# Performance work log

Measured on AMD Instinct MI355X. Metric: run time of the kernel, lower is better.

Reference implementation:

```python
import jax, jax.numpy as jnp
import numpy as np

NMS_RADIUS = 3       # conf.nms_radius (odd)
MAX_KPTS = 2048      # conf.max_num_keypoints
SUBPIXEL_TEMP = 0.5  # conf.subpixel_temp


def setup_inputs() -> dict:
    key = jax.random.key(0)
    k1, k2, k3 = jax.random.split(key, 3)
    B, H, W, C = 4, 640, 640, 64
    return {
        "keypoint_probs": jax.random.uniform(k1, (B, 1, H, W), dtype=jnp.float32),
        "raw_logits": jax.random.normal(k2, (B, 1, H, W), dtype=jnp.float32),
        "feature_map": jax.random.normal(k3, (B, C, H, W), dtype=jnp.float32),
    }


def _bilinear_sample(fm, x, y):
    # fm: (B,C,H,W); x,y: (B,N) pixel coords. F.grid_sample bilinear,
    # padding_mode='border', align_corners=True == clamp pixel coords then bilerp.
    B, C, H, W = fm.shape
    x = jnp.clip(x, 0.0, W - 1)
    y = jnp.clip(y, 0.0, H - 1)
    x0f = jnp.floor(x); y0f = jnp.floor(y)
    wx = (x - x0f)[:, None, :]
    wy = (y - y0f)[:, None, :]
    x0 = x0f.astype(jnp.int32); y0 = y0f.astype(jnp.int32)
    x1 = jnp.clip(x0 + 1, 0, W - 1); y1 = jnp.clip(y0 + 1, 0, H - 1)
    fm_flat = fm.reshape(B, C, H * W)
    bidx = jnp.arange(B)[:, None, None]
    def g(iy, ix):
        return fm_flat[bidx, jnp.arange(C)[None, :, None], (iy * W + ix)[:, None, :]]
    v00 = g(y0, x0); v01 = g(y0, x1); v10 = g(y1, x0); v11 = g(y1, x1)
    out = (v00 * (1 - wx) * (1 - wy) + v01 * wx * (1 - wy)
           + v10 * (1 - wx) * wy + v11 * wx * wy)      # (B,C,N)
    return out.transpose(0, 2, 1)                       # (B,N,C)


def reference(keypoint_probs, raw_logits, feature_map):
    B, _, H, W = keypoint_probs.shape
    r, K = NMS_RADIUS, MAX_KPTS
    pad = r // 2
    # --- NMS: keep only local maxima of the score map ---
    p = keypoint_probs[:, 0]                             # (B,H,W)
    maxp = jax.lax.reduce_window(p, -jnp.inf, jax.lax.max,
                                 (1, r, r), (1, 1, 1),
                                 ((0, 0), (pad, pad), (pad, pad)))
    nms = jnp.where(p == maxp, p, 0.0)
    # --- top-k keypoints over flattened H*W ---
    _, hw = jax.lax.top_k(nms.reshape(B, H * W), K)      # (B,K)
    h = hw // W
    w = hw % W
    kpts = jnp.stack([w, h], axis=-1).astype(jnp.float32)  # (x,y)
    # --- subpixel refinement: gather r*r patch of raw logits around each kp ---
    logits_pad = jnp.pad(raw_logits[:, 0], ((0, 0), (pad, pad), (pad, pad)))  # zero pad like nn.Unfold
    Wp = W + 2 * pad
    di, dj = jnp.meshgrid(jnp.arange(r), jnp.arange(r), indexing='ij')
    di = di.reshape(-1); dj = dj.reshape(-1)             # (r*r,)
    idx = (h[:, None, :] + di[None, :, None]) * Wp + (w[:, None, :] + dj[None, :, None])  # (B,r2,K)
    patches = logits_pad.reshape(B, -1)[jnp.arange(B)[:, None, None], idx]  # (B,r2,K)
    probs_patch = jax.nn.softmax(patches / SUBPIXEL_TEMP, axis=1)
    off = jnp.linspace(-(r - 1) / 2, (r - 1) / 2, r)
    gy, gx = jnp.meshgrid(off, off, indexing='ij')
    offsets = jnp.stack([gx, gy], axis=-1).reshape(r * r, 2).astype(jnp.float32)  # (x,y) order
    kpts = kpts + jnp.einsum('bkn,kd->bnd', probs_patch, offsets)
    # --- bilinear sample score map + descriptors at refined keypoints (one pass) ---
    stacked = jnp.concatenate([keypoint_probs, feature_map], axis=1)  # (B,1+C,H,W)
    sampled = _bilinear_sample(stacked, kpts[..., 0], kpts[..., 1])   # (B,K,1+C)
    # output: [x, y, score, desc...] per keypoint -> (B,K,2+1+C)
    return jnp.concatenate([kpts, sampled], axis=-1)
```

## Files before the change

### kernel.cpp

```cpp
#include <hip/hip_runtime.h>
#include <stdint.h>

#define B_ 4
#define H_ 640
#define W_ 640
#define C_ 64
#define K_ 2048
#define N_ (H_ * W_)
#define NBINS 131072
#define CAP 4096
#define CBLK 64
#define CHUNK (N_ / CBLK)

#define OFF_BITS   0
#define SZ_BITS    (B_ * N_ * 4)
#define OFF_HIST   (OFF_BITS + SZ_BITS)
#define SZ_HIST    (B_ * NBINS * 4)
#define OFF_CCNT   (OFF_HIST + SZ_HIST)
#define SZ_CCNT    256
#define OFF_BSTAR  (OFF_CCNT + SZ_CCNT)
#define SZ_BSTAR   16
#define OFF_CAND   (OFF_BSTAR + SZ_BSTAR)
#define SZ_CAND    (B_ * CAP * 8)
#define OFF_TOPK   (OFF_CAND + SZ_CAND)
#define SZ_TOPK    (B_ * K_ * 4)

__global__ void nms_hist_kernel(const float* __restrict__ p,
                                uint32_t* __restrict__ bits_out,
                                uint32_t* __restrict__ hist) {
    int t = blockIdx.x * blockDim.x + threadIdx.x;
    if (t >= B_ * N_) return;
    int b = t / N_;
    int i = t - b * N_;
    int y = i / W_;
    int x = i - y * W_;
    const float* pb = p + (size_t)b * N_;
    float c = pb[i];
    float m = c;
    #pragma unroll
    for (int dy = -1; dy <= 1; dy++) {
        int yy = y + dy;
        if (yy < 0 || yy >= H_) continue;
        #pragma unroll
        for (int dx = -1; dx <= 1; dx++) {
            int xx = x + dx;
            if (xx < 0 || xx >= W_) continue;
            m = fmaxf(m, pb[yy * W_ + xx]);
        }
    }
    float nms = (c == m) ? c : 0.0f;
    uint32_t bits = __float_as_uint(nms);
    bits_out[t] = bits;
    if (bits) atomicAdd(&hist[b * NBINS + (bits >> 13)], 1u);
}

__global__ __launch_bounds__(1024) void findbin_kernel(const uint32_t* __restrict__ hist,
                                                       uint32_t* __restrict__ binstar) {
    int b = blockIdx.x;
    const uint32_t* h = hist + b * NBINS;
    __shared__ uint32_t suf[1024];
    __shared__ uint32_t ssel, scum;
    int tid = threadIdx.x;
    uint32_t s = 0;
    int base = tid * 128;
    for (int j = 0; j < 128; j++) s += h[base + j];
    suf[tid] = s;
    if (tid == 0) ssel = 0xFFFFFFFFu;
    __syncthreads();
    for (int off = 1; off < 1024; off <<= 1) {
        uint32_t v = suf[tid];
        uint32_t add = (tid + off < 1024) ? suf[tid + off] : 0u;
        __syncthreads();
        suf[tid] = v + add;
        __syncthreads();
    }
    uint32_t inc = suf[tid];
    uint32_t above = inc - s;
    if (above < (uint32_t)K_ && inc >= (uint32_t)K_) { ssel = tid; scum = above; }
    __syncthreads();
    if (tid < 64) {
        uint32_t sel = ssel;
        if (sel != 0xFFFFFFFFu) {
            int b2 = sel * 128 + tid * 2;
            uint32_t c0 = h[b2], c1 = h[b2 + 1];
            uint32_t pair = c0 + c1;
            uint32_t acc = pair;
            #pragma unroll
            for (int off = 1; off < 64; off <<= 1) {
                uint32_t v = __shfl_down(acc, off);
                if (tid + off < 64) acc += v;
            }
            uint32_t aboveL = scum + (acc - pair);
            if (aboveL < (uint32_t)K_ && aboveL + pair >= (uint32_t)K_) {
                uint32_t bstar = (aboveL + c1 >= (uint32_t)K_) ? (uint32_t)(b2 + 1)
                                                               : (uint32_t)b2;
                binstar[b] = bstar;
            }
        } else if (tid == 0) {
            binstar[b] = 0;
        }
    }
}

__global__ __launch_bounds__(256) void collect_kernel(const uint32_t* __restrict__ bits_in,
                                                      const uint32_t* __restrict__ binstar,
                                                      uint32_t* __restrict__ ccnt,
                                                      unsigned long long* __restrict__ cand) {
    int b = blockIdx.x / CBLK;
    int c = blockIdx.x - b * CBLK;
    int base = b * N_ + c * CHUNK;
    uint32_t bstar = binstar[b];
    int tid = threadIdx.x;
    int lane = tid & 63, wv = tid >> 6;
    __shared__ uint32_t wtot[4];
    __shared__ uint32_t blkbase;

    uint32_t cnt = 0;
    for (int j = tid; j < CHUNK; j += 256) {
        uint32_t bits = bits_in[base + j];
        if (bits && (bits >> 13) >= bstar) cnt++;
    }
    #pragma unroll
    for (int off = 32; off > 0; off >>= 1) cnt += __shfl_down(cnt, off);
    if (lane == 0) wtot[wv] = cnt;
    __syncthreads();
    if (tid == 0) {
        uint32_t tot = wtot[0] + wtot[1] + wtot[2] + wtot[3];
        blkbase = tot ? atomicAdd(&ccnt[b * 16], tot) : 0u;
    }
    __syncthreads();
    uint32_t wbase = blkbase;
    #pragma unroll
    for (int w2 = 0; w2 < 4; w2++) if (w2 < wv) wbase += wtot[w2];

    uint32_t run = 0;
    for (int j = tid; j < CHUNK; j += 256) {
        uint32_t bits = bits_in[base + j];
        bool pass = bits && (bits >> 13) >= bstar;
        unsigned long long mask = __ballot(pass);
        if (pass) {
            uint32_t pos = wbase + run + (uint32_t)__popcll(mask & ((1ull << lane) - 1));
            int i = c * CHUNK + j;
            if (pos < CAP)
                cand[(size_t)b * CAP + pos] =
                    ((unsigned long long)bits << 32) | (unsigned long long)(0xFFFFFFFFu - (uint32_t)i);
        }
        run += (uint32_t)__popcll(mask);
    }
}

__global__ __launch_bounds__(1024) void sort_kernel(const unsigned long long* __restrict__ cand,
                                                    const uint32_t* __restrict__ ccnt,
                                                    uint32_t* __restrict__ topk) {
    __shared__ unsigned long long sh[CAP];
    int b = blockIdx.x;
    int tid = threadIdx.x;
    uint32_t cnt = ccnt[b * 16];
    if (cnt > CAP) cnt = CAP;
    const unsigned long long* cb = cand + (size_t)b * CAP;
    for (int j = tid; j < CAP; j += 1024) sh[j] = (j < (int)cnt) ? cb[j] : 0ULL;
    __syncthreads();
    for (unsigned k = 2; k <= CAP; k <<= 1) {
        for (unsigned j = k >> 1; j > 0; j >>= 1) {
            for (unsigned t = tid; t < CAP / 2; t += 1024) {
                unsigned i = (t / j) * (2 * j) + (t % j);
                unsigned ixj = i + j;
                unsigned long long a = sh[i], cc = sh[ixj];
                bool dirDesc = ((i & k) == 0);
                if (dirDesc ? (a < cc) : (a > cc)) { sh[i] = cc; sh[ixj] = a; }
            }
            __syncthreads();
        }
    }
    for (int k2 = tid; k2 < K_; k2 += 1024) {
        topk[b * K_ + k2] = 0xFFFFFFFFu - (uint32_t)(sh[k2] & 0xFFFFFFFFull);
    }
}

__global__ void final_kernel(const uint32_t* __restrict__ topk,
                             const float* __restrict__ probs,
                             const float* __restrict__ logits,
                             const float* __restrict__ fm,
                             float* __restrict__ out) {
    int gtid = blockIdx.x * blockDim.x + threadIdx.x;
    int wid = gtid >> 6;
    int lane = threadIdx.x & 63;
    if (wid >= B_ * K_) return;
    int b = wid / K_;
    int k = wid - b * K_;
    int idx = (int)topk[b * K_ + k];
    int h = idx / W_;
    int w = idx - h * W_;

    const float* lg = logits + (size_t)b * N_;
    float v[9];
    #pragma unroll
    for (int di = 0; di < 3; di++) {
        #pragma unroll
        for (int dj = 0; dj < 3; dj++) {
            int yy = h + di - 1, xx = w + dj - 1;
            float val = (yy >= 0 && yy < H_ && xx >= 0 && xx < W_) ? lg[yy * W_ + xx] : 0.0f;
            v[di * 3 + dj] = val * 2.0f;
        }
    }
    float m = v[0];
    #pragma unroll
    for (int j = 1; j < 9; j++) m = fmaxf(m, v[j]);
    float e[9], s = 0.0f;
    #pragma unroll
    for (int j = 0; j < 9; j++) { e[j] = __expf(v[j] - m); s += e[j]; }
    float inv = 1.0f / s;
    float dx = 0.0f, dy = 0.0f;
    #pragma unroll
    for (int di = 0; di < 3; di++) {
        #pragma unroll
        for (int dj = 0; dj < 3; dj++) {
            float pr = e[di * 3 + dj] * inv;
            dx += pr * (float)(dj - 1);
            dy += pr * (float)(di - 1);
        }
    }
    float x = (float)w + dx;
    float y = (float)h + dy;

    float xc = fminf(fmaxf(x, 0.0f), (float)(W_ - 1));
    float yc = fminf(fmaxf(y, 0.0f), (float)(H_ - 1));
    float x0f = floorf(xc), y0f = floorf(yc);
    float wx = xc - x0f, wy = yc - y0f;
    int x0 = (int)x0f, y0 = (int)y0f;
    int x1 = min(x0 + 1, W_ - 1), y1 = min(y0 + 1, H_ - 1);
    float w00 = (1.0f - wx) * (1.0f - wy);
    float w01 = wx * (1.0f - wy);
    float w10 = (1.0f - wx) * wy;
    float w11 = wx * wy;
    int i00 = y0 * W_ + x0, i01 = y0 * W_ + x1, i10 = y1 * W_ + x0, i11 = y1 * W_ + x1;

    float* ob = out + ((size_t)b * K_ + k) * (C_ + 3);

    const float* ch = fm + ((size_t)b * C_ + lane) * N_;
    float sv = ch[i00] * w00 + ch[i01] * w01 + ch[i10] * w10 + ch[i11] * w11;
    ob[3 + lane] = sv;

    if (lane == 0) {
        const float* pp = probs + (size_t)b * N_;
        float sp = pp[i00] * w00 + pp[i01] * w01 + pp[i10] * w10 + pp[i11] * w11;
        ob[0] = x;
        ob[1] = y;
        ob[2] = sp;
    }
}

extern "C" void kernel_launch(void* const* d_in, const int* in_sizes, int n_in,
                              void* d_out, int out_size, void* d_ws, size_t ws_size,
                              hipStream_t stream) {
    const float* probs  = (const float*)d_in[0];
    const float* logits = (const float*)d_in[1];
    const float* fm     = (const float*)d_in[2];
    float* out = (float*)d_out;

    char* ws = (char*)d_ws;
    uint32_t* bits   = (uint32_t*)(ws + OFF_BITS);
    uint32_t* hist   = (uint32_t*)(ws + OFF_HIST);
    uint32_t* ccnt   = (uint32_t*)(ws + OFF_CCNT);
    uint32_t* bstar  = (uint32_t*)(ws + OFF_BSTAR);
    unsigned long long* cand = (unsigned long long*)(ws + OFF_CAND);
    uint32_t* topk   = (uint32_t*)(ws + OFF_TOPK);

    hipMemsetAsync((void*)hist, 0, SZ_HIST + SZ_CCNT, stream);

    int total = B_ * N_;
    int blk = 256;
    nms_hist_kernel<<<(total + blk - 1) / blk, blk, 0, stream>>>(probs, bits, hist);
    findbin_kernel<<<B_, 1024, 0, stream>>>(hist, bstar);
    collect_kernel<<<B_ * CBLK, 256, 0, stream>>>(bits, bstar, ccnt, cand);
    sort_kernel<<<B_, 1024, 0, stream>>>(cand, ccnt, topk);

    int waves = B_ * K_;
    int threads = waves * 64;
    final_kernel<<<(threads + 255) / 256, 256, 0, stream>>>(topk, probs, logits, fm, out);
}
```

Measured before the change: 647.4 us.

## Vectorize NMS to four pixels per thread and restructure histogram bin search

The NMS/histogram kernel now handles four adjacent pixels per thread, reading float4 rows plus halo values and writing uint4 results. This cuts redundant neighbourhood loads and the thread count. The bin-finding kernel is rewritten as a three-level hierarchical search: segment sums read with vector loads, a wave-level scan with ballot, a 2048-bin segment staged into shared memory, then two wave scans. This replaces the serial 128-element per-thread loop and the long barrier-heavy block scan. The -1 padding sentinel is only correct because the probabilities are non-negative, and the code assumes W is divisible by four.

```diff
diff --git a/kernel.cpp b/kernel.cpp
--- a/kernel.cpp
+++ b/kernel.cpp
@@ -29,75 +29,140 @@
                                 uint32_t* __restrict__ bits_out,
                                 uint32_t* __restrict__ hist) {
     int t = blockIdx.x * blockDim.x + threadIdx.x;
-    if (t >= B_ * N_) return;
-    int b = t / N_;
-    int i = t - b * N_;
-    int y = i / W_;
-    int x = i - y * W_;
+    if (t >= B_ * N_ / 4) return;
+    int b = t / (N_ / 4);
+    int i4 = (t - b * (N_ / 4)) * 4;
+    int y = i4 / W_;
+    int x0 = i4 - y * W_;
     const float* pb = p + (size_t)b * N_;
-    float c = pb[i];
-    float m = c;
-    #pragma unroll
-    for (int dy = -1; dy <= 1; dy++) {
-        int yy = y + dy;
-        if (yy < 0 || yy >= H_) continue;
-        #pragma unroll
-        for (int dx = -1; dx <= 1; dx++) {
-            int xx = x + dx;
-            if (xx < 0 || xx >= W_) continue;
-            m = fmaxf(m, pb[yy * W_ + xx]);
-        }
-    }
-    float nms = (c == m) ? c : 0.0f;
-    uint32_t bits = __float_as_uint(nms);
-    bits_out[t] = bits;
-    if (bits) atomicAdd(&hist[b * NBINS + (bits >> 13)], 1u);
+
+    float4 rows[3];
+    float lft[3], rgt[3];
+    #pragma unroll
+    for (int r = 0; r < 3; r++) {
+        int yy = y + r - 1;
+        if (yy < 0 || yy >= H_) {
+            rows[r] = make_float4(-1.f, -1.f, -1.f, -1.f);
+            lft[r] = -1.f; rgt[r] = -1.f;
+        } else {
+            const float* rp = pb + yy * W_;
+            rows[r] = *(const float4*)(rp + x0);
+            lft[r] = (x0 > 0)       ? rp[x0 - 1] : -1.f;
+            rgt[r] = (x0 + 4 < W_)  ? rp[x0 + 4] : -1.f;
+        }
+    }
+    float m0 = -1.f, m1 = -1.f, m2 = -1.f, m3 = -1.f;
+    #pragma unroll
+    for (int r = 0; r < 3; r++) {
+        float4 v = rows[r];
+        m0 = fmaxf(m0, fmaxf(fmaxf(lft[r], v.x), v.y));
+        m1 = fmaxf(m1, fmaxf(fmaxf(v.x, v.y), v.z));
+        m2 = fmaxf(m2, fmaxf(fmaxf(v.y, v.z), v.w));
+        m3 = fmaxf(m3, fmaxf(fmaxf(v.z, v.w), rgt[r]));
+    }
+    float4 c = rows[1];
+    uint4 bits;
+    bits.x = (c.x == m0) ? __float_as_uint(c.x) : 0u;
+    bits.y = (c.y == m1) ? __float_as_uint(c.y) : 0u;
+    bits.z = (c.z == m2) ? __float_as_uint(c.z) : 0u;
+    bits.w = (c.w == m3) ? __float_as_uint(c.w) : 0u;
+    *(uint4*)(bits_out + (size_t)b * N_ + i4) = bits;
+
+    uint32_t* hb = hist + b * NBINS;
+    if (bits.x) atomicAdd(&hb[bits.x >> 13], 1u);
+    if (bits.y) atomicAdd(&hb[bits.y >> 13], 1u);
+    if (bits.z) atomicAdd(&hb[bits.z >> 13], 1u);
+    if (bits.w) atomicAdd(&hb[bits.w >> 13], 1u);
 }
 
 __global__ __launch_bounds__(1024) void findbin_kernel(const uint32_t* __restrict__ hist,
                                                        uint32_t* __restrict__ binstar) {
     int b = blockIdx.x;
     const uint32_t* h = hist + b * NBINS;
-    __shared__ uint32_t suf[1024];
-    __shared__ uint32_t ssel, scum;
+    __shared__ uint32_t segsum[64];
+    __shared__ uint32_t seg[2048];
+    __shared__ uint32_t s_sel, s_scum;
     int tid = threadIdx.x;
-    uint32_t s = 0;
-    int base = tid * 128;
-    for (int j = 0; j < 128; j++) s += h[base + j];
-    suf[tid] = s;
-    if (tid == 0) ssel = 0xFFFFFFFFu;
-    __syncthreads();
-    for (int off = 1; off < 1024; off <<= 1) {
-        uint32_t v = suf[tid];
-        uint32_t add = (tid + off < 1024) ? suf[tid + off] : 0u;
-        __syncthreads();
-        suf[tid] = v + add;
-        __syncthreads();
-    }
-    uint32_t inc = suf[tid];
-    uint32_t above = inc - s;
-    if (above < (uint32_t)K_ && inc >= (uint32_t)K_) { ssel = tid; scum = above; }
-    __syncthreads();
-    if (tid < 64) {
-        uint32_t sel = ssel;
-        if (sel != 0xFFFFFFFFu) {
-            int b2 = sel * 128 + tid * 2;
-            uint32_t c0 = h[b2], c1 = h[b2 + 1];
-            uint32_t pair = c0 + c1;
-            uint32_t acc = pair;
-            #pragma unroll
-            for (int off = 1; off < 64; off <<= 1) {
-                uint32_t v = __shfl_down(acc, off);
-                if (tid + off < 64) acc += v;
+    int lane = tid & 63, wv = tid >> 6;
+
+    #pragma unroll
+    for (int si = 0; si < 4; si++) {
+        int s = wv * 4 + si;
+        const uint32_t* sb = h + s * 2048;
+        uint32_t acc = 0;
+        #pragma unroll
+        for (int it = 0; it < 8; it++) {
+            uint4 v = *(const uint4*)(sb + (it * 64 + lane) * 4);
+            acc += v.x + v.y + v.z + v.w;
+        }
+        #pragma unroll
+        for (int off = 32; off > 0; off >>= 1) acc += __shfl_down(acc, off);
+        if (lane == 0) segsum[s] = acc;
+    }
+    __syncthreads();
+
+    if (wv == 0) {
+        uint32_t own = segsum[lane];
+        uint32_t inc = own;
+        #pragma unroll
+        for (int off = 1; off < 64; off <<= 1) {
+            uint32_t v = __shfl_down(inc, off);
+            if (lane + off < 64) inc += v;
+        }
+        uint32_t above = inc - own;
+        bool sel = (above < (uint32_t)K_) && (inc >= (uint32_t)K_);
+        unsigned long long msk = __ballot(sel);
+        if (lane == 0) {
+            if (msk == 0ULL) { s_sel = 0xFFFFFFFFu; }
+            else {
+                int s = __ffsll((long long)msk) - 1;
+                s_sel = (uint32_t)s;
             }
-            uint32_t aboveL = scum + (acc - pair);
-            if (aboveL < (uint32_t)K_ && aboveL + pair >= (uint32_t)K_) {
-                uint32_t bstar = (aboveL + c1 >= (uint32_t)K_) ? (uint32_t)(b2 + 1)
-                                                               : (uint32_t)b2;
-                binstar[b] = bstar;
-            }
-        } else if (tid == 0) {
-            binstar[b] = 0;
+        }
+        if (msk != 0ULL) {
+            int s = __ffsll((long long)msk) - 1;
+            uint32_t sc = __shfl(above, s);
+            if (lane == 0) s_scum = sc;
+        }
+    }
+    __syncthreads();
+
+    uint32_t selseg = s_sel;
+    if (selseg == 0xFFFFFFFFu) {
+        if (tid == 0) binstar[b] = 0;
+        return;
+    }
+    if (tid < 512) {
+        ((uint4*)seg)[tid] = ((const uint4*)(h + selseg * 2048))[tid];
+    }
+    __syncthreads();
+
+    if (wv == 0) {
+        uint32_t scum = s_scum;
+        uint32_t cs = 0;
+        #pragma unroll
+        for (int j = 0; j < 32; j++) cs += seg[lane * 32 + ((j + lane) & 31)];
+        uint32_t incc = cs;
+        #pragma unroll
+        for (int off = 1; off < 64; off <<= 1) {
+            uint32_t v = __shfl_down(incc, off);
+            if (lane + off < 64) incc += v;
+        }
+        uint32_t above2 = scum + (incc - cs);
+        bool sel2 = (above2 < (uint32_t)K_) && (above2 + cs >= (uint32_t)K_);
+        unsigned long long m2 = __ballot(sel2);
+        int cidx = __ffsll((long long)m2) - 1;
+        uint32_t scum2 = __shfl(above2, cidx);
+        uint32_t bv = (lane < 32) ? seg[cidx * 32 + lane] : 0u;
+        uint32_t incb = bv;
+        #pragma unroll
+        for (int off = 1; off < 32; off <<= 1) {
+            uint32_t v = __shfl_down(incb, off);
+            if (lane + off < 32) incb += v;
+        }
+        uint32_t above3 = scum2 + (incb - bv);
+        if (lane < 32 && above3 < (uint32_t)K_ && above3 + bv >= (uint32_t)K_) {
+            binstar[b] = (uint32_t)(selseg * 2048 + cidx * 32 + lane);
         }
     }
 }
@@ -268,9 +333,9 @@
 
     hipMemsetAsync((void*)hist, 0, SZ_HIST + SZ_CCNT, stream);
 
-    int total = B_ * N_;
     int blk = 256;
-    nms_hist_kernel<<<(total + blk - 1) / blk, blk, 0, stream>>>(probs, bits, hist);
+    int total4 = B_ * N_ / 4;
+    nms_hist_kernel<<<(total4 + blk - 1) / blk, blk, 0, stream>>>(probs, bits, hist);
     findbin_kernel<<<B_, 1024, 0, stream>>>(hist, bstar);
     collect_kernel<<<B_ * CBLK, 256, 0, stream>>>(bits, bstar, ccnt, cand);
     sort_kernel<<<B_, 1024, 0, stream>>>(cand, ccnt, topk);
```

New measurement: 631.0 us. -2.5%, faster.
